# Performance work log

Hardware: AMD Instinct MI355X
Metric: run time of the kernel (lower is better)

The kernel has to match this reference:

```python
import jax, jax.numpy as jnp
import numpy as np

B, C, F, T = 4, 64, 256, 256
CH = C // 2  # self.n_ch inside the module
EPS = 1e-5


def _cbp(x, W, b, g, be, m, v, a):
    # 1x1 conv == channel matmul, then BatchNorm (inference stats) + PReLU (scalar slope)
    y = jnp.einsum('oi,bift->boft', W, x) + b[None, :, None, None]
    y = (y - m[None, :, None, None]) * jax.lax.rsqrt(v[None, :, None, None] + EPS)
    y = y * g[None, :, None, None] + be[None, :, None, None]
    return jnp.where(y > 0, y, a * y)


def setup_inputs() -> dict:
    key = jax.random.key(0)
    ks = jax.random.split(key, 16)

    def conv_params(i, cin, cout, pre):
        W = jax.random.normal(ks[i], (cout, cin), dtype=jnp.float32) * 0.05
        return {
            pre + '_W': W,
            pre + '_b': jnp.zeros((cout,), jnp.float32),
            pre + '_g': jnp.ones((cout,), jnp.float32),
            pre + '_be': jnp.zeros((cout,), jnp.float32),
            pre + '_m': jax.random.normal(ks[i + 1], (cout,), dtype=jnp.float32) * 0.1,
            pre + '_v': jax.random.uniform(ks[i + 2], (cout,), dtype=jnp.float32) + 0.5,
            pre + '_a': jnp.float32(0.25),
        }

    d = {
        'inp': jax.random.normal(ks[12], (B, C, F, T), dtype=jnp.float32),
        'x': jax.random.normal(ks[13], (B, C, F, T), dtype=jnp.float32),
    }
    d.update(conv_params(0, C, 2 * CH, 'fqk'))
    d.update(conv_params(3, C, CH, 'fv'))
    d.update(conv_params(6, C, 2 * CH, 'tqk'))
    d.update(conv_params(9, CH, C, 'proj'))
    return d


def reference(inp, x,
              fqk_W, fqk_b, fqk_g, fqk_be, fqk_m, fqk_v, fqk_a,
              fv_W, fv_b, fv_g, fv_be, fv_m, fv_v, fv_a,
              tqk_W, tqk_b, tqk_g, tqk_be, tqk_m, tqk_v, tqk_a,
              proj_W, proj_b, proj_g, proj_be, proj_m, proj_v, proj_a):
    scale = 1.0 / jnp.sqrt(jnp.float32(CH))

    # frequency attention
    f_qk = _cbp(inp, fqk_W, fqk_b, fqk_g, fqk_be, fqk_m, fqk_v, fqk_a)  # B,2CH,F,T
    vf = _cbp(x, fv_W, fv_b, fv_g, fv_be, fv_m, fv_v, fv_a)             # B,CH,F,T
    r = f_qk.reshape(f_qk.shape[0], CH, 2, F, T)  # 'b (c k) f t -> b c k f t'
    qf, kf = r[:, :, 0], r[:, :, 1]
    f_score = jnp.einsum('bcft,bcyt->btfy', qf, kf) * scale
    f_score = jax.nn.softmax(f_score, axis=-1)
    fout = jnp.einsum('btfy,bcyt->bcft', f_score, vf)

    # time attention (causal mask)
    t_qk = _cbp(inp, tqk_W, tqk_b, tqk_g, tqk_be, tqk_m, tqk_v, tqk_a)
    r = t_qk.reshape(t_qk.shape[0], CH, 2, F, T)
    qt, kt = r[:, :, 0], r[:, :, 1]
    t_score = jnp.einsum('bcft,bcfy->bfty', qt, kt) * scale
    mask = jnp.triu(jnp.ones((T, T), dtype=bool), k=1)  # j - i + 1 with i == j
    neg = -jnp.finfo(t_score.dtype).max
    t_score = jnp.where(mask, neg, t_score)
    t_score = jax.nn.softmax(t_score, axis=-1)
    tout = jnp.einsum('bfty,bcfy->bcft', t_score, fout)

    out = _cbp(tout, proj_W, proj_b, proj_g, proj_be, proj_m, proj_v, proj_a)
    return out + x
```

## Files before the change

### kernel.cpp

```cpp
#include <hip/hip_runtime.h>
#include <hip/hip_bf16.h>

typedef __hip_bfloat16 bf16;
typedef __attribute__((ext_vector_type(8))) short bf16x8;
typedef __attribute__((ext_vector_type(4))) float f32x4;
typedef __attribute__((ext_vector_type(16))) float f32x16;
typedef __attribute__((ext_vector_type(8))) unsigned short u16x8;
typedef __attribute__((ext_vector_type(4))) unsigned int u32x4;
typedef __attribute__((ext_vector_type(2))) unsigned int u32x2;

struct ConvP {
  const float* W; const float* bi; const float* g; const float* be;
  const float* m; const float* v; const float* a;
};

#define QS (0.17677669529663687f * 1.4426950408889634f)

__device__ __forceinline__ int swz1024(int i) {
  return ((i & 7) << 7) | (i >> 3);
}

__device__ __forceinline__ unsigned short f2bf(float f) {
  __hip_bfloat16 h = __float2bfloat16(f);
  return __builtin_bit_cast(unsigned short, h);
}
__device__ __forceinline__ float fast_exp2(float x) {
#if __has_builtin(__builtin_amdgcn_exp2f)
  return __builtin_amdgcn_exp2f(x);
#else
  return exp2f(x);
#endif
}

__global__ __launch_bounds__(256, 2) void conv_qkv(
    const float* __restrict__ inp, const float* __restrict__ x,
    ConvP fqk, ConvP fv, ConvP tqk,
    bf16* __restrict__ Qf, bf16* __restrict__ Kf, bf16* __restrict__ Vf,
    bf16* __restrict__ Qt, bf16* __restrict__ Kt)
{
  __shared__ __attribute__((aligned(16))) unsigned short Xb[64 * 260];
  __shared__ __attribute__((aligned(16))) unsigned short S0[256 * 40];
  __shared__ __attribute__((aligned(16))) unsigned short S1[256 * 40];
  __shared__ __attribute__((aligned(8)))  float2 Pc[160];

  const int tid = threadIdx.x;
  const int b = blockIdx.x >> 8;
  const int f = blockIdx.x & 255;
  const size_t gbase = (size_t)b * 64 * 65536 + f * 256;
  const size_t tbase = (size_t)(b * 256 + f) * 8192;

  const int lane = tid & 63;
  const int wid = tid >> 6;
  const int m16 = lane & 15;
  const int quad = lane >> 4;

  if (tid < 160) {
    const ConvP& P = (tid < 64) ? fqk : (tid < 128) ? tqk : fv;
    const int o = (tid < 64) ? tid : (tid < 128) ? tid - 64 : tid - 128;
    float A = P.g[o] * rsqrtf(P.v[o] + 1e-5f);
    float B2 = (P.bi[o] - P.m[o]) * A + P.be[o];
    if (tid < 128 && ((o & 1) == 0)) { A *= QS; B2 *= QS; }
    Pc[tid] = make_float2(A, B2);
  }

  auto load_X = [&](const float* __restrict__ src) {
    #pragma unroll
    for (int r = 0; r < 16; ++r) {
      const int idx = r * 256 + tid;
      const int c = idx >> 6;
      const int t0 = (idx & 63) * 4;
      const float4 v = *(const float4*)(src + gbase + (size_t)c * 65536 + t0);
      unsigned lo = (unsigned)f2bf(v.x) | (((unsigned)f2bf(v.y)) << 16);
      unsigned hi = (unsigned)f2bf(v.z) | (((unsigned)f2bf(v.w)) << 16);
      u32x2 pk = {lo, hi};
      *(u32x2*)&Xb[c * 260 + t0] = pk;
    }
  };

  auto load_A = [&](const float* __restrict__ W, int rowbase, int ks) {
    const float* p = W + (rowbase + m16) * 64 + ks * 32 + quad * 8;
    const float4 lo = *(const float4*)p;
    const float4 hi = *(const float4*)(p + 4);
    bf16x8 r;
    r[0] = (short)f2bf(lo.x); r[1] = (short)f2bf(lo.y);
    r[2] = (short)f2bf(lo.z); r[3] = (short)f2bf(lo.w);
    r[4] = (short)f2bf(hi.x); r[5] = (short)f2bf(hi.y);
    r[6] = (short)f2bf(hi.z); r[7] = (short)f2bf(hi.w);
    return r;
  };

  auto load_B = [&](int tt, int ks) {
    const int t = tt * 16 + m16;
    const int i0 = ks * 32 + quad * 8;
    bf16x8 r;
    #pragma unroll
    for (int j = 0; j < 8; ++j) r[j] = (short)Xb[(i0 + j) * 260 + t];
    return r;
  };

  auto emit = [&](const unsigned short* S, bf16* __restrict__ dst) {
    #pragma unroll
    for (int r = 0; r < 4; ++r) {
      const int chunk = r * 256 + tid;
      const int t = chunk >> 2, part = chunk & 3;
      u32x4 v = *(const u32x4*)&S[t * 40 + part * 8];
      *(u32x4*)(dst + tbase + (size_t)chunk * 8) = v;
    }
  };

  auto leaky = [](float y, float alpha) { return y > 0.f ? y : alpha * y; };

  auto qk_pass = [&](const ConvP& P, int pcb, const bf16x8 (&Bf)[4][2]) {
    bf16x8 A[4][2];
    #pragma unroll
    for (int ot = 0; ot < 4; ++ot)
      #pragma unroll
      for (int ks = 0; ks < 2; ++ks) A[ot][ks] = load_A(P.W, ot * 16, ks);
    float pA[4][4], pB[4][4];
    #pragma unroll
    for (int ot = 0; ot < 4; ++ot)
      #pragma unroll
      for (int r = 0; r < 4; ++r) {
        const float2 pp = Pc[pcb + ot * 16 + quad * 4 + r];
        pA[ot][r] = pp.x; pB[ot][r] = pp.y;
      }
    const float alpha = P.a[0];
    #pragma unroll
    for (int i = 0; i < 4; ++i) {
      const int t = (wid * 4 + i) * 16 + m16;
      #pragma unroll
      for (int ot = 0; ot < 4; ++ot) {
        f32x4 acc = {0.f, 0.f, 0.f, 0.f};
        acc = __builtin_amdgcn_mfma_f32_16x16x32_bf16(A[ot][0], Bf[i][0], acc, 0, 0, 0);
        acc = __builtin_amdgcn_mfma_f32_16x16x32_bf16(A[ot][1], Bf[i][1], acc, 0, 0, 0);
        float y[4];
        #pragma unroll
        for (int r = 0; r < 4; ++r)
          y[r] = leaky(acc[r] * pA[ot][r] + pB[ot][r], alpha);
        const int ch0 = ot * 8 + quad * 2;
        *(unsigned*)&S0[t * 40 + ch0] = (unsigned)f2bf(y[0]) | (((unsigned)f2bf(y[2])) << 16);
        *(unsigned*)&S1[t * 40 + ch0] = (unsigned)f2bf(y[1]) | (((unsigned)f2bf(y[3])) << 16);
      }
    }
  };

  load_X(inp);
  __syncthreads();

  bf16x8 Bf[4][2];
  #pragma unroll
  for (int i = 0; i < 4; ++i)
    #pragma unroll
    for (int ks = 0; ks < 2; ++ks) Bf[i][ks] = load_B(wid * 4 + i, ks);

  qk_pass(fqk, 0, Bf);
  __syncthreads();
  emit(S0, Qf); emit(S1, Kf);
  __syncthreads();
  qk_pass(tqk, 64, Bf);
  __syncthreads();
  emit(S0, Qt); emit(S1, Kt);
  __syncthreads();
  load_X(x);
  __syncthreads();

  {
    bf16x8 A[2][2], Bv[4][2];
    #pragma unroll
    for (int i = 0; i < 4; ++i)
      #pragma unroll
      for (int ks = 0; ks < 2; ++ks) Bv[i][ks] = load_B(wid * 4 + i, ks);
    #pragma unroll
    for (int ot = 0; ot < 2; ++ot)
      #pragma unroll
      for (int ks = 0; ks < 2; ++ks) A[ot][ks] = load_A(fv.W, ot * 16, ks);
    float pA[2][4], pB[2][4];
    #pragma unroll
    for (int ot = 0; ot < 2; ++ot)
      #pragma unroll
      for (int r = 0; r < 4; ++r) {
        const float2 pp = Pc[128 + ot * 16 + quad * 4 + r];
        pA[ot][r] = pp.x; pB[ot][r] = pp.y;
      }
    const float alpha = fv.a[0];
    #pragma unroll
    for (int i = 0; i < 4; ++i) {
      const int t = (wid * 4 + i) * 16 + m16;
      #pragma unroll
      for (int ot = 0; ot < 2; ++ot) {
        f32x4 acc = {0.f, 0.f, 0.f, 0.f};
        acc = __builtin_amdgcn_mfma_f32_16x16x32_bf16(A[ot][0], Bv[i][0], acc, 0, 0, 0);
        acc = __builtin_amdgcn_mfma_f32_16x16x32_bf16(A[ot][1], Bv[i][1], acc, 0, 0, 0);
        float y[4];
        #pragma unroll
        for (int r = 0; r < 4; ++r)
          y[r] = leaky(acc[r] * pA[ot][r] + pB[ot][r], alpha);
        const int ch = ot * 16 + quad * 4;
        *(unsigned*)&S0[t * 40 + ch]     = (unsigned)f2bf(y[0]) | (((unsigned)f2bf(y[1])) << 16);
        *(unsigned*)&S0[t * 40 + ch + 2] = (unsigned)f2bf(y[2]) | (((unsigned)f2bf(y[3])) << 16);
      }
    }
  }
  __syncthreads();
  emit(S0, Vf);
}

template<bool CAUSAL>
__global__ __launch_bounds__(256, 2) void attn_k(
    const bf16* __restrict__ Qg, const bf16* __restrict__ Kg,
    const bf16* __restrict__ Vg, bf16* __restrict__ Og)
{
  __shared__ __attribute__((aligned(16))) unsigned short Kl[256 * 40];
  __shared__ __attribute__((aligned(16))) unsigned short Vt[32 * 264];
  __shared__ __attribute__((aligned(16))) unsigned short Plds[4][16 * 264];
  __shared__ __attribute__((aligned(16))) unsigned short Wsc[4][16 * 40];

  const int inst = swz1024(blockIdx.x);
  const int b = inst >> 8;
  const int s = inst & 255;
  constexpr int RS = CAUSAL ? 32 : 8192;
  const int qbase = CAUSAL ? inst * 8192 : (b * 2097152 + s * 32);

  const int tid = threadIdx.x;
  const int lane = tid & 63;
  const int wid = tid >> 6;
  const int m16 = lane & 15;
  const int quad = lane >> 4;
  const int r4 = lane >> 2, p4 = lane & 3;

  u32x4 qpre[4];
  #pragma unroll
  for (int it = 0; it < 4; ++it) {
    const int rt = wid + 4 * it;
    qpre[it] = *(const u32x4*)(Qg + qbase + (rt * 16 + r4) * RS + p4 * 8);
  }

  #pragma unroll
  for (int k2 = 0; k2 < 4; ++k2) {
    const int chunk = k2 * 256 + tid;
    const int row = chunk >> 2, part = chunk & 3;
    u32x4 val = *(const u32x4*)(Kg + qbase + row * RS + part * 8);
    *(u32x4*)&Kl[row * 40 + part * 8] = val;
  }
  if (tid < 128) {
    const unsigned short* v0 = (const unsigned short*)(Vg + qbase) + (2 * tid) * RS;
    const unsigned short* v1 = v0 + RS;
    u16x8 a[4], c[4];
    #pragma unroll
    for (int q = 0; q < 4; ++q) {
      a[q] = *(const u16x8*)(v0 + 8 * q);
      c[q] = *(const u16x8*)(v1 + 8 * q);
    }
    unsigned int* vt32 = (unsigned int*)Vt;
    #pragma unroll
    for (int cc = 0; cc < 32; ++cc) {
      unsigned lo = a[cc >> 3][cc & 7];
      unsigned hi = c[cc >> 3][cc & 7];
      vt32[(cc * 264 + 2 * tid) >> 1] = lo | (hi << 16);
    }
  }
  __syncthreads();

  unsigned short* P  = &Plds[wid][0];
  unsigned short* Ws = &Wsc[wid][0];

  bf16x8 kfr[16];
  #pragma unroll
  for (int ct = 0; ct < 16; ++ct)
    kfr[ct] = *(const bf16x8*)&Kl[(ct * 16 + m16) * 40 + quad * 8];

  #pragma unroll 1
  for (int it = 0; it < 4; ++it) {
    const int rt = wid + 4 * it;
    {
      *(u32x4*)&Ws[r4 * 40 + p4 * 8] = qpre[it];
    }
    const bf16x8 qf = *(const bf16x8*)&Ws[m16 * 40 + quad * 8];
    const int nct = CAUSAL ? (rt + 1) : 16;

    f32x4 acc[16];
    #pragma unroll
    for (int ct = 0; ct < 16; ++ct) {
      if (ct < nct) {
        f32x4 z = {0.f, 0.f, 0.f, 0.f};
        acc[ct] = __builtin_amdgcn_mfma_f32_16x16x32_bf16(kfr[ct], qf, z, 0, 0, 0);
      }
    }
    float mxr[4] = {-3e38f, -3e38f, -3e38f, -3e38f};
    #pragma unroll
    for (int ct = 0; ct < 16; ++ct) if (ct < nct) {
      #pragma unroll
      for (int r = 0; r < 4; ++r) {
        float v = acc[ct][r];
        if (CAUSAL && (ct == nct - 1) && (quad * 4 + r > m16)) v = -3e38f;
        acc[ct][r] = v;
        mxr[r] = fmaxf(mxr[r], v);
      }
    }
    float m = fmaxf(fmaxf(mxr[0], mxr[1]), fmaxf(mxr[2], mxr[3]));
    m = fmaxf(m, __shfl_xor(m, 16, 64));
    m = fmaxf(m, __shfl_xor(m, 32, 64));
    float sr[4] = {0.f, 0.f, 0.f, 0.f};
    #pragma unroll
    for (int ct = 0; ct < 16; ++ct) if (ct < nct) {
      #pragma unroll
      for (int r = 0; r < 4; ++r) {
        float p = fast_exp2(acc[ct][r] - m);
        acc[ct][r] = p;
        sr[r] += p;
      }
    }
    float ssum = (sr[0] + sr[1]) + (sr[2] + sr[3]);
    ssum += __shfl_xor(ssum, 16, 64);
    ssum += __shfl_xor(ssum, 32, 64);
    const float inv = 1.0f / ssum;

    #pragma unroll
    for (int ct = 0; ct < 16; ++ct) if (ct < nct) {
      u32x2 pk = { (unsigned)f2bf(acc[ct][0]) | (((unsigned)f2bf(acc[ct][1])) << 16),
                   (unsigned)f2bf(acc[ct][2]) | (((unsigned)f2bf(acc[ct][3])) << 16) };
      *(u32x2*)&P[m16 * 264 + ct * 16 + quad * 4] = pk;
    }
    int ksteps = CAUSAL ? ((rt >> 1) + 1) : 8;
    if (CAUSAL && ((rt & 1) == 0)) {
      u32x2 z2 = {0u, 0u};
      *(u32x2*)&P[m16 * 264 + (rt + 1) * 16 + quad * 4] = z2;
    }
    f32x4 o0 = {0.f, 0.f, 0.f, 0.f}, o1 = {0.f, 0.f, 0.f, 0.f};
    #pragma unroll
    for (int ks = 0; ks < 8; ++ks) {
      if (ks < ksteps) {
        const bf16x8 pf  = *(const bf16x8*)&P[m16 * 264 + ks * 32 + quad * 8];
        const bf16x8 vf0 = *(const bf16x8*)&Vt[m16 * 264 + ks * 32 + quad * 8];
        const bf16x8 vf1 = *(const bf16x8*)&Vt[(16 + m16) * 264 + ks * 32 + quad * 8];
        o0 = __builtin_amdgcn_mfma_f32_16x16x32_bf16(pf, vf0, o0, 0, 0, 0);
        o1 = __builtin_amdgcn_mfma_f32_16x16x32_bf16(pf, vf1, o1, 0, 0, 0);
      }
    }
    #pragma unroll
    for (int r = 0; r < 4; ++r) {
      const float invq = __shfl(inv, quad * 4 + r, 16);
      Ws[(quad * 4 + r) * 40 + m16]      = f2bf(o0[r] * invq);
      Ws[(quad * 4 + r) * 40 + 16 + m16] = f2bf(o1[r] * invq);
    }
    {
      u32x4 ov = *(const u32x4*)&Ws[r4 * 40 + p4 * 8];
      *(u32x4*)(Og + qbase + (rt * 16 + r4) * RS + p4 * 8) = ov;
    }
  }
}

__global__ __launch_bounds__(256, 2) void attn_proj(
    const bf16* __restrict__ Qg, const bf16* __restrict__ Kg,
    const bf16* __restrict__ Vg, ConvP pj,
    const float* __restrict__ x, float* __restrict__ out)
{
  __shared__ __attribute__((aligned(16))) unsigned short Kl[256 * 40];
  __shared__ __attribute__((aligned(16))) unsigned short Vt[32 * 264];
  __shared__ __attribute__((aligned(16))) unsigned short Plds[4][16 * 136];
  __shared__ __attribute__((aligned(16))) unsigned short Wsc[4][16 * 40];
  __shared__ __attribute__((aligned(16))) unsigned short Ob[256 * 40];
  __shared__ __attribute__((aligned(8)))  float2 Pc[64];

  const int inst = swz1024(blockIdx.x);
  const int b = inst >> 8;
  const int f = inst & 255;
  const int qbase = inst * 8192;

  const int tid = threadIdx.x;
  const int lane = tid & 63;
  const int wid = tid >> 6;
  const int m16 = lane & 15;
  const int quad = lane >> 4;
  const int r4 = lane >> 2, p4 = lane & 3;

  if (tid < 64) {
    const float A = pj.g[tid] * rsqrtf(pj.v[tid] + 1e-5f);
    const float B2 = (pj.bi[tid] - pj.m[tid]) * A + pj.be[tid];
    Pc[tid] = make_float2(A, B2);
  }

  u32x4 qpre[4];
  #pragma unroll
  for (int it = 0; it < 4; ++it) {
    const int rt = wid + 4 * it;
    qpre[it] = *(const u32x4*)(Qg + qbase + (rt * 16 + r4) * 32 + p4 * 8);
  }

  #pragma unroll
  for (int k2 = 0; k2 < 4; ++k2) {
    const int chunk = k2 * 256 + tid;
    const int row = chunk >> 2, part = chunk & 3;
    u32x4 val = *(const u32x4*)(Kg + qbase + row * 32 + part * 8);
    *(u32x4*)&Kl[row * 40 + part * 8] = val;
  }
  if (tid < 128) {
    const unsigned short* v0 = (const unsigned short*)(Vg + qbase) + (2 * tid) * 32;
    const unsigned short* v1 = v0 + 32;
    u16x8 a[4], c[4];
    #pragma unroll
    for (int q = 0; q < 4; ++q) {
      a[q] = *(const u16x8*)(v0 + 8 * q);
      c[q] = *(const u16x8*)(v1 + 8 * q);
    }
    unsigned int* vt32 = (unsigned int*)Vt;
    #pragma unroll
    for (int cc = 0; cc < 32; ++cc) {
      unsigned lo = a[cc >> 3][cc & 7];
      unsigned hi = c[cc >> 3][cc & 7];
      vt32[(cc * 264 + 2 * tid) >> 1] = lo | (hi << 16);
    }
  }
  __syncthreads();

  unsigned short* P  = &Plds[wid][0];
  unsigned short* Ws = &Wsc[wid][0];

  bf16x8 kfr[16];
  #pragma unroll
  for (int ct = 0; ct < 16; ++ct)
    kfr[ct] = *(const bf16x8*)&Kl[(ct * 16 + m16) * 40 + quad * 8];

  #pragma unroll 1
  for (int it = 0; it < 4; ++it) {
    const int rt = wid + 4 * it;
    {
      *(u32x4*)&Ws[r4 * 40 + p4 * 8] = qpre[it];
    }
    const bf16x8 qf = *(const bf16x8*)&Ws[m16 * 40 + quad * 8];
    const int nct = rt + 1;

    f32x4 acc[16];
    #pragma unroll
    for (int ct = 0; ct < 16; ++ct) {
      if (ct < nct) {
        f32x4 z = {0.f, 0.f, 0.f, 0.f};
        acc[ct] = __builtin_amdgcn_mfma_f32_16x16x32_bf16(kfr[ct], qf, z, 0, 0, 0);
      }
    }
    float mxr[4] = {-3e38f, -3e38f, -3e38f, -3e38f};
    #pragma unroll
    for (int ct = 0; ct < 16; ++ct) if (ct < nct) {
      #pragma unroll
      for (int r = 0; r < 4; ++r) {
        float v = acc[ct][r];
        if ((ct == nct - 1) && (quad * 4 + r > m16)) v = -3e38f;
        acc[ct][r] = v;
        mxr[r] = fmaxf(mxr[r], v);
      }
    }
    float m = fmaxf(fmaxf(mxr[0], mxr[1]), fmaxf(mxr[2], mxr[3]));
    m = fmaxf(m, __shfl_xor(m, 16, 64));
    m = fmaxf(m, __shfl_xor(m, 32, 64));
    float sr[4] = {0.f, 0.f, 0.f, 0.f};
    #pragma unroll
    for (int ct = 0; ct < 16; ++ct) if (ct < nct) {
      #pragma unroll
      for (int r = 0; r < 4; ++r) {
        float p = fast_exp2(acc[ct][r] - m);
        acc[ct][r] = p;
        sr[r] += p;
      }
    }
    float ssum = (sr[0] + sr[1]) + (sr[2] + sr[3]);
    ssum += __shfl_xor(ssum, 16, 64);
    ssum += __shfl_xor(ssum, 32, 64);
    const float inv = 1.0f / ssum;

    const int ksteps = (rt >> 1) + 1;
    f32x4 o0 = {0.f, 0.f, 0.f, 0.f}, o1 = {0.f, 0.f, 0.f, 0.f};
    #pragma unroll
    for (int hh = 0; hh < 2; ++hh) {
      if (8 * hh < nct) {
        #pragma unroll
        for (int c2 = 0; c2 < 8; ++c2) {
          const int ct = 8 * hh + c2;
          if (ct < nct) {
            u32x2 pk = { (unsigned)f2bf(acc[ct][0]) | (((unsigned)f2bf(acc[ct][1])) << 16),
                         (unsigned)f2bf(acc[ct][2]) | (((unsigned)f2bf(acc[ct][3])) << 16) };
            *(u32x2*)&P[m16 * 136 + c2 * 16 + quad * 4] = pk;
          }
        }
        if (((rt & 1) == 0) && (((rt + 1) >> 3) == hh)) {
          u32x2 z2 = {0u, 0u};
          *(u32x2*)&P[m16 * 136 + ((rt + 1) & 7) * 16 + quad * 4] = z2;
        }
        #pragma unroll
        for (int k4 = 0; k4 < 4; ++k4) {
          const int ks = 4 * hh + k4;
          if (ks < ksteps) {
            const bf16x8 pf  = *(const bf16x8*)&P[m16 * 136 + k4 * 32 + quad * 8];
            const bf16x8 vf0 = *(const bf16x8*)&Vt[m16 * 264 + ks * 32 + quad * 8];
            const bf16x8 vf1 = *(const bf16x8*)&Vt[(16 + m16) * 264 + ks * 32 + quad * 8];
            o0 = __builtin_amdgcn_mfma_f32_16x16x32_bf16(pf, vf0, o0, 0, 0, 0);
            o1 = __builtin_amdgcn_mfma_f32_16x16x32_bf16(pf, vf1, o1, 0, 0, 0);
          }
        }
      }
    }
    #pragma unroll
    for (int r = 0; r < 4; ++r) {
      const float invq = __shfl(inv, quad * 4 + r, 16);
      const int row = rt * 16 + quad * 4 + r;
      Ob[row * 40 + m16]      = f2bf(o0[r] * invq);
      Ob[row * 40 + 16 + m16] = f2bf(o1[r] * invq);
    }
  }
  __syncthreads();

  {
    const int n32 = lane & 31;
    const int kh = lane >> 5;
    bf16x8 Afr[2][2];
    #pragma unroll
    for (int ot = 0; ot < 2; ++ot)
      #pragma unroll
      for (int ks = 0; ks < 2; ++ks) {
        const float* p = pj.W + (ot * 32 + n32) * 32 + ks * 16 + kh * 8;
        const float4 lo = *(const float4*)p;
        const float4 hi = *(const float4*)(p + 4);
        bf16x8 r;
        r[0] = (short)f2bf(lo.x); r[1] = (short)f2bf(lo.y);
        r[2] = (short)f2bf(lo.z); r[3] = (short)f2bf(lo.w);
        r[4] = (short)f2bf(hi.x); r[5] = (short)f2bf(hi.y);
        r[6] = (short)f2bf(hi.z); r[7] = (short)f2bf(hi.w);
        Afr[ot][ks] = r;
      }
    const float alpha = pj.a[0];
    const size_t gbase = (size_t)b * 64 * 65536 + f * 256;

    #pragma unroll
    for (int tt = 0; tt < 2; ++tt) {
      const int t = wid * 64 + tt * 32 + n32;
      const bf16x8 B0 = *(const bf16x8*)&Ob[t * 40 + 0 * 16 + kh * 8];
      const bf16x8 B1 = *(const bf16x8*)&Ob[t * 40 + 1 * 16 + kh * 8];
      #pragma unroll
      for (int ot = 0; ot < 2; ++ot) {
        f32x16 acc = {};
        acc = __builtin_amdgcn_mfma_f32_32x32x16_bf16(Afr[ot][0], B0, acc, 0, 0, 0);
        acc = __builtin_amdgcn_mfma_f32_32x32x16_bf16(Afr[ot][1], B1, acc, 0, 0, 0);
        #pragma unroll
        for (int reg = 0; reg < 16; ++reg) {
          const int o = ot * 32 + (reg & 3) + 8 * (reg >> 2) + 4 * kh;
          const float2 pp = Pc[o];
          float y = acc[reg] * pp.x + pp.y;
          y = y > 0.f ? y : alpha * y;
          const size_t off = gbase + (size_t)o * 65536 + t;
          out[off] = y + x[off];
        }
      }
    }
  }
}

extern "C" void kernel_launch(void* const* d_in, const int* in_sizes, int n_in,
                              void* d_out, int out_size, void* d_ws, size_t ws_size,
                              hipStream_t stream) {
  const float* inp = (const float*)d_in[0];
  const float* x   = (const float*)d_in[1];
  auto cp = [&](int i) {
    return ConvP{ (const float*)d_in[i],     (const float*)d_in[i + 1],
                  (const float*)d_in[i + 2], (const float*)d_in[i + 3],
                  (const float*)d_in[i + 4], (const float*)d_in[i + 5],
                  (const float*)d_in[i + 6] };
  };
  ConvP fqk = cp(2), fv = cp(9), tqk = cp(16), pj = cp(23);

  char* ws = (char*)d_ws;
  const size_t SZ = (size_t)4 * 256 * 256 * 32 * 2;
  bf16* Qf = (bf16*)(ws + 0 * SZ);
  bf16* Kf = (bf16*)(ws + 1 * SZ);
  bf16* Vf = (bf16*)(ws + 2 * SZ);
  bf16* Qt = (bf16*)(ws + 3 * SZ);
  bf16* Kt = (bf16*)(ws + 4 * SZ);
  bf16* Ft = (bf16*)(ws + 5 * SZ);

  conv_qkv<<<1024, 256, 0, stream>>>(inp, x, fqk, fv, tqk, Qf, Kf, Vf, Qt, Kt);
  attn_k<false><<<1024, 256, 0, stream>>>(Qf, Kf, Vf, Ft);
  attn_proj<<<1024, 256, 0, stream>>>(Qt, Kt, Ft, pj, x, (float*)d_out);
}
```

Before: 309.7 us.

## Specialize frequency attention kernel for higher occupancy with halved P staging

Replaces the templated attention kernel with a non-causal-only version that targets three blocks per SM instead of two. It shrinks shared memory by staging P in two halves of 128 columns, and reuses the P buffer for the Q and output scratch. It keeps only half the K fragments in registers and reloads the rest from LDS on each iteration. The aim is more concurrent waves to hide latency, at the cost of extra LDS traffic and register pressure that could force spills.

```diff
diff --git a/kernel.cpp b/kernel.cpp
--- a/kernel.cpp
+++ b/kernel.cpp
@@ -205,21 +205,19 @@
   emit(S0, Vf);
 }
 
-template<bool CAUSAL>
-__global__ __launch_bounds__(256, 2) void attn_k(
+__global__ __launch_bounds__(256, 3) void attn_f(
     const bf16* __restrict__ Qg, const bf16* __restrict__ Kg,
     const bf16* __restrict__ Vg, bf16* __restrict__ Og)
 {
   __shared__ __attribute__((aligned(16))) unsigned short Kl[256 * 40];
   __shared__ __attribute__((aligned(16))) unsigned short Vt[32 * 264];
-  __shared__ __attribute__((aligned(16))) unsigned short Plds[4][16 * 264];
-  __shared__ __attribute__((aligned(16))) unsigned short Wsc[4][16 * 40];
+  __shared__ __attribute__((aligned(16))) unsigned short Plds[4][16 * 132];
 
   const int inst = swz1024(blockIdx.x);
   const int b = inst >> 8;
   const int s = inst & 255;
-  constexpr int RS = CAUSAL ? 32 : 8192;
-  const int qbase = CAUSAL ? inst * 8192 : (b * 2097152 + s * 32);
+  const int RS = 8192;
+  const int qbase = b * 2097152 + s * 32;
 
   const int tid = threadIdx.x;
   const int lane = tid & 63;
@@ -261,76 +259,65 @@
   }
   __syncthreads();
 
-  unsigned short* P  = &Plds[wid][0];
-  unsigned short* Ws = &Wsc[wid][0];
-
-  bf16x8 kfr[16];
-  #pragma unroll
-  for (int ct = 0; ct < 16; ++ct)
+  unsigned short* P = &Plds[wid][0];
+
+  bf16x8 kfr[8];
+  #pragma unroll
+  for (int ct = 0; ct < 8; ++ct)
     kfr[ct] = *(const bf16x8*)&Kl[(ct * 16 + m16) * 40 + quad * 8];
 
   #pragma unroll 1
   for (int it = 0; it < 4; ++it) {
     const int rt = wid + 4 * it;
     {
-      *(u32x4*)&Ws[r4 * 40 + p4 * 8] = qpre[it];
-    }
-    const bf16x8 qf = *(const bf16x8*)&Ws[m16 * 40 + quad * 8];
-    const int nct = CAUSAL ? (rt + 1) : 16;
+      *(u32x4*)&P[r4 * 40 + p4 * 8] = qpre[it];
+    }
+    const bf16x8 qf = *(const bf16x8*)&P[m16 * 40 + quad * 8];
 
     f32x4 acc[16];
     #pragma unroll
     for (int ct = 0; ct < 16; ++ct) {
-      if (ct < nct) {
-        f32x4 z = {0.f, 0.f, 0.f, 0.f};
-        acc[ct] = __builtin_amdgcn_mfma_f32_16x16x32_bf16(kfr[ct], qf, z, 0, 0, 0);
-      }
+      f32x4 z = {0.f, 0.f, 0.f, 0.f};
+      const bf16x8 kf = (ct < 8) ? kfr[ct]
+          : *(const bf16x8*)&Kl[(ct * 16 + m16) * 40 + quad * 8];
+      acc[ct] = __builtin_amdgcn_mfma_f32_16x16x32_bf16(kf, qf, z, 0, 0, 0);
     }
     float mxr[4] = {-3e38f, -3e38f, -3e38f, -3e38f};
     #pragma unroll
-    for (int ct = 0; ct < 16; ++ct) if (ct < nct) {
-      #pragma unroll
-      for (int r = 0; r < 4; ++r) {
-        float v = acc[ct][r];
-        if (CAUSAL && (ct == nct - 1) && (quad * 4 + r > m16)) v = -3e38f;
-        acc[ct][r] = v;
-        mxr[r] = fmaxf(mxr[r], v);
-      }
-    }
+    for (int ct = 0; ct < 16; ++ct)
+      #pragma unroll
+      for (int r = 0; r < 4; ++r) mxr[r] = fmaxf(mxr[r], acc[ct][r]);
     float m = fmaxf(fmaxf(mxr[0], mxr[1]), fmaxf(mxr[2], mxr[3]));
     m = fmaxf(m, __shfl_xor(m, 16, 64));
     m = fmaxf(m, __shfl_xor(m, 32, 64));
     float sr[4] = {0.f, 0.f, 0.f, 0.f};
     #pragma unroll
-    for (int ct = 0; ct < 16; ++ct) if (ct < nct) {
+    for (int ct = 0; ct < 16; ++ct)
       #pragma unroll
       for (int r = 0; r < 4; ++r) {
         float p = fast_exp2(acc[ct][r] - m);
         acc[ct][r] = p;
         sr[r] += p;
       }
-    }
     float ssum = (sr[0] + sr[1]) + (sr[2] + sr[3]);
     ssum += __shfl_xor(ssum, 16, 64);
     ssum += __shfl_xor(ssum, 32, 64);
     const float inv = 1.0f / ssum;
 
-    #pragma unroll
-    for (int ct = 0; ct < 16; ++ct) if (ct < nct) {
-      u32x2 pk = { (unsigned)f2bf(acc[ct][0]) | (((unsigned)f2bf(acc[ct][1])) << 16),
-                   (unsigned)f2bf(acc[ct][2]) | (((unsigned)f2bf(acc[ct][3])) << 16) };
-      *(u32x2*)&P[m16 * 264 + ct * 16 + quad * 4] = pk;
-    }
-    int ksteps = CAUSAL ? ((rt >> 1) + 1) : 8;
-    if (CAUSAL && ((rt & 1) == 0)) {
-      u32x2 z2 = {0u, 0u};
-      *(u32x2*)&P[m16 * 264 + (rt + 1) * 16 + quad * 4] = z2;
-    }
     f32x4 o0 = {0.f, 0.f, 0.f, 0.f}, o1 = {0.f, 0.f, 0.f, 0.f};
     #pragma unroll
-    for (int ks = 0; ks < 8; ++ks) {
-      if (ks < ksteps) {
-        const bf16x8 pf  = *(const bf16x8*)&P[m16 * 264 + ks * 32 + quad * 8];
+    for (int hh = 0; hh < 2; ++hh) {
+      #pragma unroll
+      for (int c2 = 0; c2 < 8; ++c2) {
+        const int ct = 8 * hh + c2;
+        u32x2 pk = { (unsigned)f2bf(acc[ct][0]) | (((unsigned)f2bf(acc[ct][1])) << 16),
+                     (unsigned)f2bf(acc[ct][2]) | (((unsigned)f2bf(acc[ct][3])) << 16) };
+        *(u32x2*)&P[m16 * 132 + c2 * 16 + quad * 4] = pk;
+      }
+      #pragma unroll
+      for (int k4 = 0; k4 < 4; ++k4) {
+        const int ks = 4 * hh + k4;
+        const bf16x8 pf  = *(const bf16x8*)&P[m16 * 132 + k4 * 32 + quad * 8];
         const bf16x8 vf0 = *(const bf16x8*)&Vt[m16 * 264 + ks * 32 + quad * 8];
         const bf16x8 vf1 = *(const bf16x8*)&Vt[(16 + m16) * 264 + ks * 32 + quad * 8];
         o0 = __builtin_amdgcn_mfma_f32_16x16x32_bf16(pf, vf0, o0, 0, 0, 0);
@@ -340,11 +327,11 @@
     #pragma unroll
     for (int r = 0; r < 4; ++r) {
       const float invq = __shfl(inv, quad * 4 + r, 16);
-      Ws[(quad * 4 + r) * 40 + m16]      = f2bf(o0[r] * invq);
-      Ws[(quad * 4 + r) * 40 + 16 + m16] = f2bf(o1[r] * invq);
+      P[(quad * 4 + r) * 40 + m16]      = f2bf(o0[r] * invq);
+      P[(quad * 4 + r) * 40 + 16 + m16] = f2bf(o1[r] * invq);
     }
     {
-      u32x4 ov = *(const u32x4*)&Ws[r4 * 40 + p4 * 8];
+      u32x4 ov = *(const u32x4*)&P[r4 * 40 + p4 * 8];
       *(u32x4*)(Og + qbase + (rt * 16 + r4) * RS + p4 * 8) = ov;
     }
   }
@@ -576,6 +563,6 @@
   bf16* Ft = (bf16*)(ws + 5 * SZ);
 
   conv_qkv<<<1024, 256, 0, stream>>>(inp, x, fqk, fv, tqk, Qf, Kf, Vf, Qt, Kt);
-  attn_k<false><<<1024, 256, 0, stream>>>(Qf, Kf, Vf, Ft);
+  attn_f<<<1024, 256, 0, stream>>>(Qf, Kf, Vf, Ft);
   attn_proj<<<1024, 256, 0, stream>>>(Qt, Kt, Ft, pj, x, (float*)d_out);
 }
```

Measured after the change: 377.1 us. +21.8%, slower.
